# Kernel optimization log

Hardware: AMD Instinct MI355X
Metric: run time of the kernel (lower is better)

## Reference

```python
import jax, jax.numpy as jnp
import numpy as np


def setup_inputs() -> dict:
    key = jax.random.key(0)
    k1, k2, k3, k4, k5 = jax.random.split(key, 5)
    B, S, K, N, G = 4, 2048, 4096, 4096, 64  # G = group_size -> num_groups = K // G = 64
    x = jax.random.normal(k1, (B, S, K), dtype=jnp.float32)
    # int2 codes stored one-per-int8 slot (low 2 bits valid); use int32 container
    weight_q = jax.random.randint(k2, (N, K), 0, 4, dtype=jnp.int32)
    scale = jax.random.uniform(k3, (N, K // G), dtype=jnp.float32) * 0.05 + 0.01
    zp = jax.random.uniform(k4, (N, K // G), dtype=jnp.float32) * 3.0
    bias = jax.random.normal(k5, (N,), dtype=jnp.float32)
    return {"x": x, "weight_q": weight_q, "scale": scale, "zp": zp, "bias": bias}


def _dequant(weight_q, scale, zp):
    # weight_q: [N, K] int codes in [0,4); scale/zp: [N, num_groups]
    N, K = weight_q.shape
    num_groups = scale.shape[1]
    gs = K // num_groups  # group_size
    q = weight_q.astype(jnp.float32).reshape(N, num_groups, gs)
    w = (q - zp[:, :, None]) * scale[:, :, None]
    return w.reshape(N, K)


def reference(x, weight_q, scale, zp, bias):
    # asymm_qw2_gemm: out = x @ dequant(W)^T + bias
    w = _dequant(weight_q, scale, zp)            # [N, K]
    out = jnp.einsum('bsk,nk->bsn', x, w)        # [B, S, N]
    return out + bias
```

## Files before the change

kernel.cpp:

```cpp
#include <hip/hip_runtime.h>
#include <stdint.h>


typedef __attribute__((ext_vector_type(4))) float  f32x4;
typedef __attribute__((ext_vector_type(4))) int    i32x4;
typedef __attribute__((ext_vector_type(8))) __bf16 bf16x8;
typedef __attribute__((ext_vector_type(4))) unsigned short u16x4;

__device__ __forceinline__ unsigned short f2bf(float f) {
  unsigned u = __builtin_bit_cast(unsigned, f);
  u += 0x7fffu + ((u >> 16) & 1u);
  return (unsigned short)(u >> 16);
}

__device__ __forceinline__ void async16(const void* g, void* l) {
  __builtin_amdgcn_global_load_lds(
      (const __attribute__((address_space(1))) unsigned int*)g,
      (__attribute__((address_space(3))) unsigned int*)l, 16, 0, 0);
}

__global__ __launch_bounds__(256) void prep_kernel(
    const float* __restrict__ x, unsigned short* __restrict__ xb, int xchunks,
    const int* __restrict__ wq, const float* __restrict__ scale,
    const float* __restrict__ zp, unsigned short* __restrict__ wb,
    int wchunks, int K, int G) {
  int xblocks = (xchunks + 255) >> 8;
  if ((int)blockIdx.x < xblocks) {
    int i = blockIdx.x * 256 + threadIdx.x;
    if (i >= xchunks) return;
    f32x4 a = ((const f32x4*)x)[i];
    u16x4 o;
    o[0] = f2bf(a[0]); o[1] = f2bf(a[1]); o[2] = f2bf(a[2]); o[3] = f2bf(a[3]);
    *(u16x4*)(xb + (size_t)i * 4) = o;
  } else {
    int i = (blockIdx.x - xblocks) * 256 + threadIdx.x;
    if (i >= wchunks) return;
    int k4 = i * 4;
    int n = k4 / K, kk = k4 % K;
    int ng = K / G;
    int g = kk / G;
    float s = scale[(size_t)n * ng + g];
    float b = -zp[(size_t)n * ng + g] * s;
    i32x4 qv = ((const i32x4*)wq)[i];
    u16x4 o;
    o[0] = f2bf((float)qv[0] * s + b); o[1] = f2bf((float)qv[1] * s + b);
    o[2] = f2bf((float)qv[2] * s + b); o[3] = f2bf((float)qv[3] * s + b);
    *(u16x4*)(wb + (size_t)i * 4) = o;
  }
}

#define BM 128
#define BN 128
#define BK 32

__global__ __launch_bounds__(256, 2) void gemm_bt_kernel(
    const unsigned short* __restrict__ A,
    const unsigned short* __restrict__ B,
    const float* __restrict__ bias,
    float* __restrict__ C, int M, int N, int K) {
  __shared__ unsigned short As[BM * BK];
  __shared__ unsigned short Bs[BN * BK];

  const int tid  = threadIdx.x;
  const int lane = tid & 63;
  const int wave = tid >> 6;
  const int wm = wave >> 1, wn = wave & 1;
  const int q = lane >> 4, r = lane & 15;
  const int m0 = blockIdx.y * BM;
  const int n0 = blockIdx.x * BN;

  const int srow = tid >> 2, schunk = tid & 3;
  const int gchunk = schunk ^ ((srow >> 1) & 3);
  const unsigned short* aG0 = A + (size_t)(m0 + srow) * K      + gchunk * 8;
  const unsigned short* aG1 = A + (size_t)(m0 + 64 + srow) * K + gchunk * 8;
  const unsigned short* bG0 = B + (size_t)(n0 + srow) * K      + gchunk * 8;
  const unsigned short* bG1 = B + (size_t)(n0 + 64 + srow) * K + gchunk * 8;
  unsigned short* aL0 = &As[tid * 8];
  unsigned short* aL1 = &As[2048 + tid * 8];
  unsigned short* bL0 = &Bs[tid * 8];
  unsigned short* bL1 = &Bs[2048 + tid * 8];

  const int qc = (q ^ ((r >> 1) & 3)) * 8;

  f32x4 acc[4][4] = {};

#pragma unroll 1
  for (int kk = 0; kk < K; kk += BK) {
    async16(aG0 + kk, aL0);
    async16(aG1 + kk, aL1);
    async16(bG0 + kk, bL0);
    async16(bG1 + kk, bL1);
    __syncthreads();

    bf16x8 af[4], bf[4];
#pragma unroll
    for (int i = 0; i < 4; ++i) {
      af[i] = *(const bf16x8*)&As[(wm * 64 + i * 16 + r) * BK + qc];
      bf[i] = *(const bf16x8*)&Bs[(wn * 64 + i * 16 + r) * BK + qc];
    }
#pragma unroll
    for (int i = 0; i < 4; ++i)
#pragma unroll
      for (int j = 0; j < 4; ++j)
        acc[i][j] = __builtin_amdgcn_mfma_f32_16x16x32_bf16(af[i], bf[j], acc[i][j], 0, 0, 0);
    __syncthreads();
  }

  float bv[4];
#pragma unroll
  for (int j = 0; j < 4; ++j) bv[j] = bias[n0 + wn * 64 + j * 16 + r];
#pragma unroll
  for (int i = 0; i < 4; ++i) {
    int mbase = m0 + wm * 64 + i * 16 + q * 4;
#pragma unroll
    for (int e = 0; e < 4; ++e) {
      float* crow = C + (size_t)(mbase + e) * N + n0 + wn * 64 + r;
#pragma unroll
      for (int j = 0; j < 4; ++j)
        crow[j * 16] = acc[i][j][e] + bv[j];
    }
  }
}

__global__ __launch_bounds__(256) void naive_kernel(
    const float* __restrict__ x, const int* __restrict__ wq,
    const float* __restrict__ scale, const float* __restrict__ zp,
    const float* __restrict__ bias, float* __restrict__ out,
    int M, int N, int K, int G) {
  int idx = blockIdx.x * 256 + threadIdx.x;
  if (idx >= M * N) return;
  int m = idx / N, n = idx % N;
  const float* xr = x + (size_t)m * K;
  const int* wr = wq + (size_t)n * K;
  int ng = K / G;
  float acc = 0.f;
  for (int g = 0; g < ng; ++g) {
    float s = scale[(size_t)n * ng + g];
    float b = -zp[(size_t)n * ng + g] * s;
    for (int k = 0; k < G; ++k)
      acc += xr[g * G + k] * ((float)wr[g * G + k] * s + b);
  }
  out[idx] = acc + bias[n];
}

extern "C" void kernel_launch(void* const* d_in, const int* in_sizes, int n_in,
                              void* d_out, int out_size, void* d_ws, size_t ws_size,
                              hipStream_t stream) {
  const float* x     = (const float*)d_in[0];
  const int*   wq    = (const int*)d_in[1];
  const float* scale = (const float*)d_in[2];
  const float* zp    = (const float*)d_in[3];
  const float* bias  = (const float*)d_in[4];
  float* out = (float*)d_out;

  const int N  = in_sizes[4];
  const int K  = in_sizes[1] / N;
  const int ng = in_sizes[2] / N;
  const int G  = K / ng;
  const int M  = in_sizes[0] / K;

  size_t xb_bytes = (size_t)M * K * 2;
  size_t wb_bytes = (size_t)N * K * 2;
  if (ws_size < xb_bytes + wb_bytes) {
    int total = M * N;
    naive_kernel<<<dim3((total + 255) / 256), dim3(256), 0, stream>>>(
        x, wq, scale, zp, bias, out, M, N, K, G);
    return;
  }

  unsigned short* xb = (unsigned short*)d_ws;
  unsigned short* wb = (unsigned short*)((char*)d_ws + xb_bytes);

  int xchunks = M * K / 4;
  int wchunks = N * K / 4;
  int xblocks = (xchunks + 255) / 256;
  int wblocks = (wchunks + 255) / 256;
  prep_kernel<<<dim3(xblocks + wblocks), dim3(256), 0, stream>>>(
      x, xb, xchunks, wq, scale, zp, wb, wchunks, K, G);

  dim3 grid(N / BN, M / BM);
  gemm_bt_kernel<<<grid, dim3(256), 0, stream>>>(xb, wb, bias, out, M, N, K);
}
```

Before: 560.3 us.

## Enlarge GEMM tile to 256x256 with 4-stage async LDS pipeline

Changes the bf16 GEMM to 256x256 tiles with 512 threads (8 waves, each computing 128x64). It adds a 4-buffer async global-to-LDS prefetch ring with explicit vmcnt waits, s_setprio around the MFMA blocks, and a 1D grid remapped for XCD locality. The aim is to hide global-load latency and raise arithmetic intensity per tile. In exchange it uses more LDS (128 KB per block) and more accumulator registers, so occupancy may drop.

Result: slower. 622.0 us (+11.0%).

```diff
diff --git a/kernel.cpp b/kernel.cpp
--- a/kernel.cpp
+++ b/kernel.cpp
@@ -49,69 +49,108 @@
   }
 }
 
-#define BM 128
-#define BN 128
+#define BM 256
+#define BN 256
 #define BK 32
-
-__global__ __launch_bounds__(256, 2) void gemm_bt_kernel(
+#define NBUF 4
+
+__global__ __launch_bounds__(512, 2) void gemm_bt_kernel(
     const unsigned short* __restrict__ A,
     const unsigned short* __restrict__ B,
     const float* __restrict__ bias,
     float* __restrict__ C, int M, int N, int K) {
-  __shared__ unsigned short As[BM * BK];
-  __shared__ unsigned short Bs[BN * BK];
+  __shared__ unsigned short As[NBUF * BM * BK];
+  __shared__ unsigned short Bs[NBUF * BM * BK];
 
   const int tid  = threadIdx.x;
   const int lane = tid & 63;
   const int wave = tid >> 6;
-  const int wm = wave >> 1, wn = wave & 1;
+  const int wm = wave >> 2, wn = wave & 3;
   const int q = lane >> 4, r = lane & 15;
-  const int m0 = blockIdx.y * BM;
-  const int n0 = blockIdx.x * BN;
-
-  const int srow = tid >> 2, schunk = tid & 3;
-  const int gchunk = schunk ^ ((srow >> 1) & 3);
-  const unsigned short* aG0 = A + (size_t)(m0 + srow) * K      + gchunk * 8;
-  const unsigned short* aG1 = A + (size_t)(m0 + 64 + srow) * K + gchunk * 8;
-  const unsigned short* bG0 = B + (size_t)(n0 + srow) * K      + gchunk * 8;
-  const unsigned short* bG1 = B + (size_t)(n0 + 64 + srow) * K + gchunk * 8;
-  unsigned short* aL0 = &As[tid * 8];
-  unsigned short* aL1 = &As[2048 + tid * 8];
-  unsigned short* bL0 = &Bs[tid * 8];
-  unsigned short* bL1 = &Bs[2048 + tid * 8];
-
-  const int qc = (q ^ ((r >> 1) & 3)) * 8;
-
-  f32x4 acc[4][4] = {};
+
+  int id = blockIdx.x;
+  {
+    int nwg = gridDim.x;
+    if ((nwg & 7) == 0) id = (id & 7) * (nwg >> 3) + (id >> 3);
+  }
+  const int nbx = N / BN;
+  const int m0 = (id / nbx) * BM;
+  const int n0 = (id % nbx) * BN;
+
+  const int srow = tid >> 2;
+  const int gch  = (tid & 3) ^ ((tid >> 3) & 3);
+  const unsigned short* aG = A + (size_t)(m0 + srow) * K + gch * 8;
+  const unsigned short* bG = B + (size_t)(n0 + srow) * K + gch * 8;
+  const size_t rowblk = (size_t)128 * K;
+
+  const int s0   = (q ^ ((r >> 1) & 3)) * 8;
+  const int aOff = (wm * 128 + r) * BK + s0;
+  const int bOff = (wn * 64  + r) * BK + s0;
+
+  f32x4 acc[8][4] = {};
+  const int NT = K / BK;
+
+#define STAGE(bi, kk) { \
+    unsigned short* al = As + (bi) * (BM * BK) + tid * 8; \
+    unsigned short* bl = Bs + (bi) * (BM * BK) + tid * 8; \
+    async16(aG + (kk), al);  async16(aG + rowblk + (kk), al + 4096); \
+    async16(bG + (kk), bl);  async16(bG + rowblk + (kk), bl + 4096); }
+
+  STAGE(0, 0)
+  if (NT > 1) STAGE(1, BK)
+  if (NT > 2) STAGE(2, 2 * BK)
 
 #pragma unroll 1
-  for (int kk = 0; kk < K; kk += BK) {
-    async16(aG0 + kk, aL0);
-    async16(aG1 + kk, aL1);
-    async16(bG0 + kk, bL0);
-    async16(bG1 + kk, bL1);
-    __syncthreads();
-
-    bf16x8 af[4], bf[4];
-#pragma unroll
-    for (int i = 0; i < 4; ++i) {
-      af[i] = *(const bf16x8*)&As[(wm * 64 + i * 16 + r) * BK + qc];
-      bf[i] = *(const bf16x8*)&Bs[(wn * 64 + i * 16 + r) * BK + qc];
-    }
+  for (int t = 0; t < NT; ++t) {
+    if (t + 3 < NT) STAGE((t + 3) & 3, (t + 3) * BK)
+    if (t + 3 < NT)      asm volatile("s_waitcnt vmcnt(12)" ::: "memory");
+    else if (t + 2 < NT) asm volatile("s_waitcnt vmcnt(8)"  ::: "memory");
+    else if (t + 1 < NT) asm volatile("s_waitcnt vmcnt(4)"  ::: "memory");
+    else                 asm volatile("s_waitcnt vmcnt(0)"  ::: "memory");
+    __builtin_amdgcn_s_barrier();
+    asm volatile("" ::: "memory");
+
+    const int base = (t & 3) * (BM * BK);
+    bf16x8 bfr[4], af0[4], af1[4];
+#pragma unroll
+    for (int j = 0; j < 4; ++j)
+      bfr[j] = *(const bf16x8*)&Bs[base + bOff + j * 16 * BK];
+#pragma unroll
+    for (int i = 0; i < 4; ++i)
+      af0[i] = *(const bf16x8*)&As[base + aOff + i * 16 * BK];
+
+    __builtin_amdgcn_s_setprio(1);
 #pragma unroll
     for (int i = 0; i < 4; ++i)
 #pragma unroll
       for (int j = 0; j < 4; ++j)
-        acc[i][j] = __builtin_amdgcn_mfma_f32_16x16x32_bf16(af[i], bf[j], acc[i][j], 0, 0, 0);
-    __syncthreads();
+        acc[i][j] = __builtin_amdgcn_mfma_f32_16x16x32_bf16(
+            af0[i], bfr[j], acc[i][j], 0, 0, 0);
+    __builtin_amdgcn_s_setprio(0);
+
+#pragma unroll
+    for (int i = 0; i < 4; ++i)
+      af1[i] = *(const bf16x8*)&As[base + aOff + (4 + i) * 16 * BK];
+
+    __builtin_amdgcn_s_setprio(1);
+#pragma unroll
+    for (int i = 0; i < 4; ++i)
+#pragma unroll
+      for (int j = 0; j < 4; ++j)
+        acc[4 + i][j] = __builtin_amdgcn_mfma_f32_16x16x32_bf16(
+            af1[i], bfr[j], acc[4 + i][j], 0, 0, 0);
+    __builtin_amdgcn_s_setprio(0);
+
+    asm volatile("" ::: "memory");
+    __builtin_amdgcn_s_barrier();
   }
 
   float bv[4];
 #pragma unroll
   for (int j = 0; j < 4; ++j) bv[j] = bias[n0 + wn * 64 + j * 16 + r];
 #pragma unroll
-  for (int i = 0; i < 4; ++i) {
-    int mbase = m0 + wm * 64 + i * 16 + q * 4;
+  for (int i = 0; i < 8; ++i) {
+    int mbase = m0 + wm * 128 + i * 16 + q * 4;
 #pragma unroll
     for (int e = 0; e < 4; ++e) {
       float* crow = C + (size_t)(mbase + e) * N + n0 + wn * 64 + r;
@@ -161,7 +200,8 @@
 
   size_t xb_bytes = (size_t)M * K * 2;
   size_t wb_bytes = (size_t)N * K * 2;
-  if (ws_size < xb_bytes + wb_bytes) {
+  bool divisible = (M % BM == 0) && (N % BN == 0) && (K % BK == 0);
+  if (ws_size < xb_bytes + wb_bytes || !divisible) {
     int total = M * N;
     naive_kernel<<<dim3((total + 255) / 256), dim3(256), 0, stream>>>(
         x, wq, scale, zp, bias, out, M, N, K, G);
@@ -178,6 +218,6 @@
   prep_kernel<<<dim3(xblocks + wblocks), dim3(256), 0, stream>>>(
       x, xb, xchunks, wq, scale, zp, wb, wchunks, K, G);
 
-  dim3 grid(N / BN, M / BM);
-  gemm_bt_kernel<<<grid, dim3(256), 0, stream>>>(xb, wb, bias, out, M, N, K);
-}
+  dim3 grid((M / BM) * (N / BN));
+  gemm_bt_kernel<<<grid, dim3(512), 0, stream>>>(xb, wb, bias, out, M, N, K);
+}
```
